# Kernel optimization log

Measured on AMD Instinct MI355X. Metric: run time of the kernel, lower is better.

The kernel has to match this reference:

```python
import jax, jax.numpy as jnp
import numpy as np

N = 50000   # nodes
F = 32      # num_node_features
EMB = 32    # embedding_size
R = 8       # num_relations
L = 5       # num_layers
E = 400000  # edges


def setup_inputs() -> dict:
    key = jax.random.key(0)
    ks = jax.random.split(key, 12)
    s = 0.1  # weight scale ~ 1/sqrt(fan_in) for stability over 5 residual layers
    return {
        "x": jax.random.normal(ks[0], (N, F), jnp.float32),
        "edge_index": jax.random.randint(ks[1], (2, E), 0, N, jnp.int32),
        "edge_type": jax.random.randint(ks[2], (E,), 0, R, jnp.int32),
        "edge_dist": jax.random.uniform(ks[3], (E,), jnp.float32),
        "fc_W": jax.random.normal(ks[4], (F, EMB), jnp.float32) * s,
        "fc_b": jnp.zeros((EMB,), jnp.float32),
        "rgcn_W": jax.random.normal(ks[5], (L, R, EMB, EMB), jnp.float32) * s,
        "rgcn_root": jax.random.normal(ks[6], (L, EMB, EMB), jnp.float32) * s,
        "rgcn_bias": jnp.zeros((L, EMB), jnp.float32),
        "mlp_W1": jax.random.normal(ks[7], (1 + R, EMB), jnp.float32) * s,
        "mlp_b1": jnp.zeros((EMB,), jnp.float32),
        "mlp_W2": jax.random.normal(ks[8], (EMB, EMB * EMB), jnp.float32) * s,
        "mlp_b2": jnp.zeros((EMB * EMB,), jnp.float32),
        "nn_root": jax.random.normal(ks[9], (L, EMB, EMB), jnp.float32) * s,
        "nn_bias": jnp.zeros((L, EMB), jnp.float32),
    }


def _forward(x, edge_index, edge_type, edge_dist, fc_W, fc_b, rgcn_W, rgcn_root,
             rgcn_bias, mlp_W1, mlp_b1, mlp_W2, mlp_b2, nn_root, nn_bias):
    n = x.shape[0]
    src, dst = edge_index[0], edge_index[1]  # source_to_target flow

    # edge_attr_c = [distance, onehot(edge_type)] : [E, 1+R]
    onehot = jax.nn.one_hot(edge_type, R, dtype=x.dtype)
    eattr = jnp.concatenate([edge_dist[:, None], onehot], axis=1)

    # Shared edge_mlp -> per-edge [EMB, EMB] weight (same for every NNConv layer)
    We = (jax.nn.relu(eattr @ mlp_W1 + mlp_b1) @ mlp_W2 + mlp_b2).reshape(-1, EMB, EMB)

    # degree for NNConv mean aggregation
    deg = jax.ops.segment_sum(jnp.ones_like(edge_dist), dst, num_segments=n)
    denom = jnp.maximum(deg, 1.0)[:, None]

    # per-relation in-degree for RGCN per-relation mean
    rel_cnt = []
    for r in range(R):
        c = jax.ops.segment_sum((edge_type == r).astype(x.dtype), dst, num_segments=n)
        rel_cnt.append(jnp.maximum(c, 1.0)[:, None])

    h = jax.nn.relu(x @ fc_W + fc_b)
    for l in range(L):
        # RGCNConv: root transform + per-relation mean of W_r x_j
        out = h @ rgcn_root[l] + rgcn_bias[l]
        for r in range(R):
            mask_r = (edge_type == r).astype(h.dtype)[:, None]
            msg = (h @ rgcn_W[l, r])[src] * mask_r  # [E, EMB]
            out = out + jax.ops.segment_sum(msg, dst, num_segments=n) / rel_cnt[r]
        h_disc = jax.nn.relu(out)

        # NNConv: x_j @ Theta(e) per edge, mean-aggregated, + root + bias
        msg = jnp.einsum('ei,eio->eo', h[src], We)  # [E, EMB]
        agg = jax.ops.segment_sum(msg, dst, num_segments=n) / denom
        h_cont = jax.nn.relu(h @ nn_root[l] + agg + nn_bias[l])

        h = h + h_disc + h_cont
    return h


def reference(x, edge_index, edge_type, edge_dist, fc_W, fc_b, rgcn_W, rgcn_root,
              rgcn_bias, mlp_W1, mlp_b1, mlp_W2, mlp_b2, nn_root, nn_bias):
    return _forward(x, edge_index, edge_type, edge_dist, fc_W, fc_b, rgcn_W,
                    rgcn_root, rgcn_bias, mlp_W1, mlp_b1, mlp_W2, mlp_b2,
                    nn_root, nn_bias)
```

## Files before the change

### kernel.cpp

```cpp
#include <hip/hip_runtime.h>

#define N_NODES 50000
#define N_EDGES 400000
#define EMB 32
#define NREL 8
#define NLAYER 5
#define NPB 16
#define NBLK (N_NODES / NPB)
#define KROWS 43
#define NCHUNK 196
#define E2CAP (N_EDGES + 8 * N_NODES)

typedef __attribute__((ext_vector_type(8))) short short8;
typedef __attribute__((ext_vector_type(4))) float f32x4;
typedef __attribute__((ext_vector_type(4))) unsigned int u32x4v;

__device__ __forceinline__ unsigned short f2bf(float f) {
    unsigned u = __float_as_uint(f);
    unsigned r = u + 0x7FFF + ((u >> 16) & 1);
    return (unsigned short)(r >> 16);
}

__device__ __forceinline__ unsigned cvt_pk(float a, float b) {
    unsigned r;
    asm("v_cvt_pk_bf16_f32 %0, %1, %2" : "=v"(r) : "v"(a), "v"(b));
    return r;
}

__device__ __forceinline__ int pdeg_of(int d) {
    return (d > 0 ? d + 7 : 8) & ~7;
}


__global__ __launch_bounds__(256) void fill_kernel(int* __restrict__ zeroblk,
                                                   float* __restrict__ ha,
                                                   float* __restrict__ hb,
                                                   unsigned* __restrict__ hb16a,
                                                   unsigned* __restrict__ hb16b) {
    int i = blockIdx.x * 256 + threadIdx.x;
    if (i < 10 * N_NODES) zeroblk[i] = 0;
    if (i < EMB) { ha[(size_t)N_NODES * EMB + i] = 0.0f; hb[(size_t)N_NODES * EMB + i] = 0.0f; }
    if (i < EMB / 2) {
        hb16a[(size_t)N_NODES * (EMB / 2) + i] = 0u;
        hb16b[(size_t)N_NODES * (EMB / 2) + i] = 0u;
    }
}

__global__ __launch_bounds__(256) void hist_kernel(const int* __restrict__ ei,
                                                   const int* __restrict__ et,
                                                   int* __restrict__ deg,
                                                   int* __restrict__ relcnt) {
    int e = blockIdx.x * 256 + threadIdx.x;
    if (e < N_EDGES) {
        int d = ei[N_EDGES + e];
        atomicAdd(&deg[d], 1);
        atomicAdd(&relcnt[d * NREL + et[e]], 1);
    }
}

__global__ __launch_bounds__(256) void nodeprep_kernel(const int* __restrict__ deg,
                                                       const int* __restrict__ relcnt,
                                                       int* __restrict__ bsum,
                                                       float* __restrict__ invdeg,
                                                       float* __restrict__ invcnt,
                                                       unsigned char* __restrict__ perm) {
    __shared__ int wsum[4];
    int tid = threadIdx.x, lane = tid & 63, wv = tid >> 6;
    int i = blockIdx.x * 256 + tid;
    int d = (i < N_NODES) ? deg[i] : 0;
    int v = (i < N_NODES) ? pdeg_of(d) : 0;
    #pragma unroll
    for (int off = 32; off > 0; off >>= 1) v += __shfl_down(v, off, 64);
    if (lane == 0) wsum[wv] = v;
    __syncthreads();
    if (tid == 0) bsum[blockIdx.x] = wsum[0] + wsum[1] + wsum[2] + wsum[3];
    if (i < N_NODES) {
        invdeg[i] = 1.0f / (float)(d > 0 ? d : 1);
        #pragma unroll
        for (int r = 0; r < NREL; r++) {
            int c = relcnt[i * NREL + r];
            invcnt[i * NREL + r] = 1.0f / (float)(c > 0 ? c : 1);
        }
    }
    if (i < NBLK) {
        int dd[NPB]; unsigned char idx[NPB];
        #pragma unroll
        for (int k = 0; k < NPB; k++) { dd[k] = deg[i * NPB + k]; idx[k] = (unsigned char)k; }
        for (int a = 1; a < NPB; a++) {
            int dv = dd[a]; unsigned char iv = idx[a];
            int j = a - 1;
            while (j >= 0 && dd[j] < dv) { dd[j + 1] = dd[j]; idx[j + 1] = idx[j]; j--; }
            dd[j + 1] = dv; idx[j + 1] = iv;
        }
        #pragma unroll
        for (int k = 0; k < NPB; k++) perm[i * NPB + k] = idx[k];
    }
}

__global__ __launch_bounds__(256) void boff_kernel(const int* __restrict__ bsum,
                                                   int* __restrict__ boff,
                                                   int* __restrict__ row_ptr) {
    __shared__ int ws[4];
    int tid = threadIdx.x, lane = tid & 63, w = tid >> 6;
    int v = (tid < NCHUNK) ? bsum[tid] : 0;
    int incl = v;
    #pragma unroll
    for (int off = 1; off < 64; off <<= 1) {
        int t = __shfl_up(incl, off, 64);
        if (lane >= off) incl += t;
    }
    if (lane == 63) ws[w] = incl;
    __syncthreads();
    int add = 0;
    for (int j = 0; j < w; j++) add += ws[j];
    if (tid < NCHUNK) boff[tid] = add + incl - v;
    if (tid == 0) row_ptr[N_NODES] = ws[0] + ws[1] + ws[2] + ws[3];
}

__global__ __launch_bounds__(256) void rptr_kernel(const int* __restrict__ deg,
                                                   const int* __restrict__ boff,
                                                   int* __restrict__ row_ptr) {
    __shared__ int ws[4];
    int tid = threadIdx.x, lane = tid & 63, w = tid >> 6;
    int i = blockIdx.x * 256 + tid;
    int v = (i < N_NODES) ? pdeg_of(deg[i]) : 0;
    int incl = v;
    #pragma unroll
    for (int off = 1; off < 64; off <<= 1) {
        int t = __shfl_up(incl, off, 64);
        if (lane >= off) incl += t;
    }
    if (lane == 63) ws[w] = incl;
    __syncthreads();
    int add = boff[blockIdx.x];
    for (int j = 0; j < w; j++) add += ws[j];
    if (i < N_NODES) row_ptr[i] = add + incl - v;
}

__global__ __launch_bounds__(256) void scatter_kernel(const int* __restrict__ ei,
                                                      const int* __restrict__ et,
                                                      const float* __restrict__ ed,
                                                      const int* __restrict__ row_ptr,
                                                      const int* __restrict__ deg,
                                                      int* __restrict__ cursor,
                                                      int2* __restrict__ edge2,
                                                      const unsigned char* __restrict__ perm,
                                                      int4* __restrict__ wavetab) {
    int e = blockIdx.x * 256 + threadIdx.x;
    if (e < N_EDGES) {
        int d = ei[N_EDGES + e];
        int pos = row_ptr[d] + atomicAdd(&cursor[d], 1);
        edge2[pos] = make_int2(ei[e] | (et[e] << 16), __float_as_int(ed[e]));
    }
    if (e < N_NODES) {
        int base = row_ptr[e], d = deg[e], pd = pdeg_of(d);
        for (int p = base + d; p < base + pd; ++p)
            edge2[p] = make_int2(N_NODES, 0);
    }
    if (e < NBLK * 8) {
        int b = e >> 3, wv = e & 7;
        int s0 = perm[b * NPB + wv], s1 = perm[b * NPB + (NPB - 1 - wv)];
        int nA = b * NPB + s0, nB = b * NPB + s1;
        int pb0 = row_ptr[nA], pd0 = row_ptr[nA + 1] - pb0;
        int pb1 = row_ptr[nB], pd1 = row_ptr[nB + 1] - pb1;
        wavetab[e] = make_int4(s0 | (s1 << 8), pb0, pb1, pd0 | (pd1 << 16));
    }
}

__global__ __launch_bounds__(256) void wtbf_kernel(const float* __restrict__ W2,
                                                   const float* __restrict__ b2,
                                                   const float* __restrict__ rgcnW,
                                                   const float* __restrict__ rgcnRoot,
                                                   const float* __restrict__ nnRoot,
                                                   unsigned short* __restrict__ WB) {
    int m = blockIdx.x;
    const float* src;
    if (m < 32) src = W2 + (size_t)m * 1024;
    else if (m == 32) src = b2;
    else {
        int t = m - 33, l = t / 10, j = t % 10;
        src = (j < 8) ? rgcnW + (size_t)(l * 8 + j) * 1024
            : (j == 8) ? rgcnRoot + (size_t)l * 1024
                       : nnRoot + (size_t)l * 1024;
    }
    unsigned short* dst = WB + (size_t)m * 1024;
    #pragma unroll
    for (int c = 0; c < 4; c++) {
        int idx = c * 256 + threadIdx.x;
        int o = idx >> 5, k = idx & 31;
        int i = (k >> 1) + ((k & 1) << 4);
        dst[o * 32 + k] = f2bf(src[i * 32 + o]);
    }
}


__global__ __launch_bounds__(256) void fc_kernel(const float* __restrict__ x,
                                                 const float* __restrict__ W,
                                                 const float* __restrict__ b,
                                                 float* __restrict__ h,
                                                 unsigned short* __restrict__ hb16) {
    __shared__ __align__(16) float xt[8][EMB];
    int tid = threadIdx.x;
    int nl = tid >> 5, lane = tid & 31;
    int n0 = blockIdx.x * 8;
    xt[tid >> 5][tid & 31] = x[n0 * EMB + tid];
    __syncthreads();
    float acc = b[lane];
    #pragma unroll
    for (int i = 0; i < EMB; i++) acc += xt[nl][i] * W[i * EMB + lane];
    float v = fmaxf(acc, 0.0f);
    int ol = ((lane & 15) << 1) | (lane >> 4);
    h[(size_t)(n0 + nl) * EMB + ol] = v;
    float pv = __shfl_down(v, 16, 32);
    unsigned pk = cvt_pk(v, pv);
    if (lane < 16)
        *(unsigned*)&hb16[(size_t)(n0 + nl) * EMB + 2 * lane] = pk;
}


__device__ __forceinline__ void gath(const unsigned short* __restrict__ hb16, int4 E, int m,
                                     unsigned& uA, unsigned& uB) {
    uA = *(const unsigned*)(hb16 + (((size_t)(E.x & 0xFFFF)) << 5) + 2 * m);
    uB = *(const unsigned*)(hb16 + (((size_t)(E.z & 0xFFFF)) << 5) + 2 * m);
}

__device__ __forceinline__ void proc_pair(int4 E, unsigned uA, unsigned uB,
                                          const float2* wrb2f, float w10_0, float w10_1,
                                          unsigned selm, int m,
                                          unsigned& A0s, unsigned& A1s, unsigned& ASs,
                                          unsigned& B0s, unsigned& B1s) {
    int ra = (E.x >> 16) & 7, rb = (E.z >> 16) & 7;
    float2 wa = wrb2f[ra * 16 + m];
    float2 wb = wrb2f[rb * 16 + m];
    float da = __int_as_float(E.y), db = __int_as_float(E.w);
    float hA0 = fmaxf(fmaf(da, w10_0, wa.x), 0.f);
    float hA1 = fmaxf(fmaf(da, w10_1, wa.y), 0.f);
    float hB0 = fmaxf(fmaf(db, w10_0, wb.x), 0.f);
    float hB1 = fmaxf(fmaf(db, w10_1, wb.y), 0.f);
    A0s = cvt_pk(hA0, hB0);
    A1s = cvt_pk(hA1, hB1);
    ASs = cvt_pk((float)((selm >> ra) & 1u), (float)((selm >> rb) & 1u));
    B0s = (uA & 0xFFFFu) | (uB << 16);
    B1s = (uA >> 16) | (uB & 0xFFFF0000u);
}

__device__ __forceinline__ void mfma6(const unsigned* fa0v, const unsigned* fa1v,
                                      const unsigned* fasv, const unsigned* fb0v,
                                      const unsigned* fb1v,
                                      f32x4& aP00, f32x4& aP01, f32x4& aP10, f32x4& aP11,
                                      f32x4& aS0, f32x4& aS1) {
    u32x4v u0 = {fa0v[0], fa0v[1], fa0v[2], fa0v[3]};
    u32x4v u1 = {fa1v[0], fa1v[1], fa1v[2], fa1v[3]};
    u32x4v us = {fasv[0], fasv[1], fasv[2], fasv[3]};
    u32x4v v0 = {fb0v[0], fb0v[1], fb0v[2], fb0v[3]};
    u32x4v v1 = {fb1v[0], fb1v[1], fb1v[2], fb1v[3]};
    short8 A0 = __builtin_bit_cast(short8, u0);
    short8 A1 = __builtin_bit_cast(short8, u1);
    short8 AS = __builtin_bit_cast(short8, us);
    short8 B0 = __builtin_bit_cast(short8, v0);
    short8 B1 = __builtin_bit_cast(short8, v1);
    aP00 = __builtin_amdgcn_mfma_f32_16x16x32_bf16(A0, B0, aP00, 0, 0, 0);
    aP01 = __builtin_amdgcn_mfma_f32_16x16x32_bf16(A0, B1, aP01, 0, 0, 0);
    aP10 = __builtin_amdgcn_mfma_f32_16x16x32_bf16(A1, B0, aP10, 0, 0, 0);
    aP11 = __builtin_amdgcn_mfma_f32_16x16x32_bf16(A1, B1, aP11, 0, 0, 0);
    aS0  = __builtin_amdgcn_mfma_f32_16x16x32_bf16(AS, B0, aS0, 0, 0, 0);
    aS1  = __builtin_amdgcn_mfma_f32_16x16x32_bf16(AS, B1, aS1, 0, 0, 0);
}

__device__ __forceinline__ void edge_pass(const unsigned short* __restrict__ hb16,
                                          const int2* __restrict__ edge2,
                                          const float2* wrb2f,
                                          int pb, int pe, int quad, int m,
                                          float w10_0, float w10_1, unsigned selm,
                                          int4 E0, unsigned u0A, unsigned u0B,
                                          f32x4& aP00, f32x4& aP01, f32x4& aP10,
                                          f32x4& aP11, f32x4& aS0, f32x4& aS1) {
    {
        unsigned fa0v[4] = {0,0,0,0}, fa1v[4] = {0,0,0,0}, fasv[4] = {0,0,0,0};
        unsigned fb0v[4] = {0,0,0,0}, fb1v[4] = {0,0,0,0};
        proc_pair(E0, u0A, u0B, wrb2f, w10_0, w10_1, selm, m,
                  fa0v[0], fa1v[0], fasv[0], fb0v[0], fb1v[0]);
        if (pb + 8 < pe) {
            int4 E = *(const int4*)&edge2[pb + 8 + quad * 2];
            unsigned uA, uB; gath(hb16, E, m, uA, uB);
            proc_pair(E, uA, uB, wrb2f, w10_0, w10_1, selm, m,
                      fa0v[1], fa1v[1], fasv[1], fb0v[1], fb1v[1]);
        }
        if (pb + 16 < pe) {
            int4 E = *(const int4*)&edge2[pb + 16 + quad * 2];
            unsigned uA, uB; gath(hb16, E, m, uA, uB);
            proc_pair(E, uA, uB, wrb2f, w10_0, w10_1, selm, m,
                      fa0v[2], fa1v[2], fasv[2], fb0v[2], fb1v[2]);
        }
        if (pb + 24 < pe) {
            int4 E = *(const int4*)&edge2[pb + 24 + quad * 2];
            unsigned uA, uB; gath(hb16, E, m, uA, uB);
            proc_pair(E, uA, uB, wrb2f, w10_0, w10_1, selm, m,
                      fa0v[3], fa1v[3], fasv[3], fb0v[3], fb1v[3]);
        }
        mfma6(fa0v, fa1v, fasv, fb0v, fb1v, aP00, aP01, aP10, aP11, aS0, aS1);
    }
    for (int c0 = pb + 32; c0 < pe; c0 += 32) {
        unsigned fa0v[4] = {0,0,0,0}, fa1v[4] = {0,0,0,0}, fasv[4] = {0,0,0,0};
        unsigned fb0v[4] = {0,0,0,0}, fb1v[4] = {0,0,0,0};
        #pragma unroll
        for (int jp = 0; jp < 4; ++jp) {
            if (c0 + jp * 8 < pe) {
                int4 E = *(const int4*)&edge2[c0 + jp * 8 + quad * 2];
                unsigned uA, uB; gath(hb16, E, m, uA, uB);
                proc_pair(E, uA, uB, wrb2f, w10_0, w10_1, selm, m,
                          fa0v[jp], fa1v[jp], fasv[jp], fb0v[jp], fb1v[jp]);
            }
        }
        mfma6(fa0v, fa1v, fasv, fb0v, fb1v, aP00, aP01, aP10, aP11, aS0, aS1);
    }
}

__device__ __forceinline__ void stage_node(unsigned short* __restrict__ P, int quad, int m,
                                           float idg, const float* __restrict__ invcnt_n,
                                           const unsigned short* __restrict__ hb16row,
                                           const f32x4& aP00, const f32x4& aP01,
                                           const f32x4& aP10, const f32x4& aP11,
                                           const f32x4& aS0, const f32x4& aS1) {
    #pragma unroll
    for (int reg = 0; reg < 4; ++reg) {
        const int row = quad * 4 + reg;
        *(unsigned*)&P[row * EMB + 2 * m]        = cvt_pk(aP00[reg] * idg, aP01[reg] * idg);
        *(unsigned*)&P[(row + 16) * EMB + 2 * m] = cvt_pk(aP10[reg] * idg, aP11[reg] * idg);
        if (row <= 8) {
            const float sc = (row == 0) ? idg : invcnt_n[row - 1];
            *(unsigned*)&P[(32 + row) * EMB + 2 * m] = cvt_pk(aS0[reg] * sc, aS1[reg] * sc);
        }
    }
    if (quad < 2) {
        unsigned hh = *(const unsigned*)(hb16row + 2 * m);
        *(unsigned*)&P[(41 + quad) * EMB + 2 * m] = hh;
    }
}

__global__ __launch_bounds__(512, 6) void layer_kernel(
    const float* __restrict__ h,
    const unsigned short* __restrict__ hb16,
    const int2* __restrict__ edge2,
    const int4* __restrict__ wavetab,
    const float* __restrict__ invdeg,
    const float* __restrict__ invcnt,
    const float* __restrict__ W1,
    const float* __restrict__ b1,
    const unsigned short* __restrict__ WBs,
    const unsigned short* __restrict__ WBl,
    const float* __restrict__ rgcnBias_l,
    const float* __restrict__ nnBias_l,
    float* __restrict__ hout,
    unsigned short* __restrict__ hb16out,
    int last)
{
    __shared__ __align__(16) unsigned short P_lds[NPB * KROWS * EMB];
    __shared__ __align__(16) float2 wrb2f[NREL * 16];

    const int tid = threadIdx.x;
    const int n0 = blockIdx.x * NPB;

    if (tid < 128) {
        int r = tid >> 4, mi = tid & 15;
        wrb2f[r * 16 + mi] = make_float2(W1[(1 + r) * EMB + mi] + b1[mi],
                                         W1[(1 + r) * EMB + mi + 16] + b1[mi + 16]);
    }

    const int l    = tid & 63;
    const int w    = tid >> 6;
    const int quad = l >> 4;
    const int m    = l & 15;
    const float w10_0 = W1[m];
    const float w10_1 = W1[m + 16];
    const unsigned selm = (m == 0) ? 0xFFu : (m <= 8 ? (1u << (m - 1)) : 0u);

    int4 wt = wavetab[blockIdx.x * 8 + w];
    const int hw0 = wt.x & 0xFF, hw1 = (wt.x >> 8) & 0xFF;
    const int pb0 = wt.y, pe0 = wt.y + (wt.w & 0xFFFF);
    const int pb1 = wt.z, pe1 = wt.z + (int)((unsigned)wt.w >> 16);
    int4 E0 = *(const int4*)&edge2[pb0 + quad * 2];
    int4 E1 = *(const int4*)&edge2[pb1 + quad * 2];
    unsigned u0A, u0B, u1A, u1B;
    gath(hb16, E0, m, u0A, u0B);
    gath(hb16, E1, m, u1A, u1B);

    __syncthreads();

    {
        f32x4 aP00 = {0,0,0,0}, aP01 = {0,0,0,0}, aP10 = {0,0,0,0}, aP11 = {0,0,0,0};
        f32x4 aS0 = {0,0,0,0}, aS1 = {0,0,0,0};
        edge_pass(hb16, edge2, wrb2f, pb0, pe0, quad, m, w10_0, w10_1, selm,
                  E0, u0A, u0B, aP00, aP01, aP10, aP11, aS0, aS1);
        const int n = n0 + hw0;
        stage_node(P_lds + (size_t)hw0 * KROWS * EMB, quad, m, invdeg[n],
                   invcnt + (size_t)n * NREL, hb16 + (size_t)n * EMB,
                   aP00, aP01, aP10, aP11, aS0, aS1);
    }
    {
        f32x4 aP00 = {0,0,0,0}, aP01 = {0,0,0,0}, aP10 = {0,0,0,0}, aP11 = {0,0,0,0};
        f32x4 aS0 = {0,0,0,0}, aS1 = {0,0,0,0};
        edge_pass(hb16, edge2, wrb2f, pb1, pe1, quad, m, w10_0, w10_1, selm,
                  E1, u1A, u1B, aP00, aP01, aP10, aP11, aS0, aS1);
        const int n = n0 + hw1;
        stage_node(P_lds + (size_t)hw1 * KROWS * EMB, quad, m, invdeg[n],
                   invcnt + (size_t)n * NREL, hb16 + (size_t)n * EMB,
                   aP00, aP01, aP10, aP11, aS0, aS1);
    }
    __syncthreads();

    const int node16 = l & 15;
    const int o0 = l & 15;

    f32x4 accN0 = {0,0,0,0}, accN1 = {0,0,0,0};
    f32x4 accR0 = {0,0,0,0}, accR1 = {0,0,0,0};

    #pragma unroll
    for (int j = 0; j < 6; j++) {
        const int rr = w + 8 * j;
        if (rr < KROWS) {
            const unsigned short* Bsrc = (rr < 33) ? (WBs + (size_t)rr * 1024)
                                                   : (WBl + (size_t)(rr - 33) * 1024);
            short8 bf0 = *(const short8*)(Bsrc + o0 * 32 + quad * 8);
            short8 bf1 = *(const short8*)(Bsrc + (o0 + 16) * 32 + quad * 8);
            short8 a = *(const short8*)&P_lds[(size_t)node16 * KROWS * EMB + rr * EMB + quad * 8];
            if (rr <= 32 || rr == 42) {
                accN0 = __builtin_amdgcn_mfma_f32_16x16x32_bf16(a, bf0, accN0, 0, 0, 0);
                accN1 = __builtin_amdgcn_mfma_f32_16x16x32_bf16(a, bf1, accN1, 0, 0, 0);
            } else {
                accR0 = __builtin_amdgcn_mfma_f32_16x16x32_bf16(a, bf0, accR0, 0, 0, 0);
                accR1 = __builtin_amdgcn_mfma_f32_16x16x32_bf16(a, bf1, accR1, 0, 0, 0);
            }
        }
    }
    __syncthreads();

    float* RedAll = (float*)&P_lds[0];
    {
        float* my = RedAll + w * 1024;
        #pragma unroll
        for (int reg = 0; reg < 4; reg++) {
            int nd = quad * 4 + reg;
            my[nd * 32 + o0]            = accN0[reg];
            my[nd * 32 + o0 + 16]       = accN1[reg];
            my[512 + nd * 32 + o0]      = accR0[reg];
            my[512 + nd * 32 + o0 + 16] = accR1[reg];
        }
    }
    __syncthreads();

    {
        const int hw2 = tid >> 5, lane = tid & 31;
        const int n2 = n0 + hw2;
        float sn = 0.0f, sr = 0.0f;
        #pragma unroll
        for (int ww = 0; ww < 8; ww++) {
            sn += RedAll[ww * 1024 + tid];
            sr += RedAll[ww * 1024 + 512 + tid];
        }
        const int il = ((lane & 15) << 1) | (lane >> 4);
        float hd = h[(size_t)n2 * EMB + il];
        float o_r = fmaxf(sr + rgcnBias_l[lane], 0.0f);
        float o_n = fmaxf(sn + nnBias_l[lane], 0.0f);
        float outv = hd + o_r + o_n;
        hout[(size_t)n2 * EMB + (last ? lane : il)] = outv;
        if (!last) {
            float pv = __shfl_down(outv, 16, 32);
            unsigned pk = cvt_pk(outv, pv);
            if (lane < 16)
                *(unsigned*)&hb16out[(size_t)n2 * EMB + 2 * lane] = pk;
        }
    }
}


extern "C" void kernel_launch(void* const* d_in, const int* in_sizes, int n_in,
                              void* d_out, int out_size, void* d_ws, size_t ws_size,
                              hipStream_t stream) {
    const float* x        = (const float*)d_in[0];
    const int*   ei       = (const int*)d_in[1];
    const int*   et       = (const int*)d_in[2];
    const float* ed       = (const float*)d_in[3];
    const float* fcW      = (const float*)d_in[4];
    const float* fcb      = (const float*)d_in[5];
    const float* rgcnW    = (const float*)d_in[6];
    const float* rgcnRoot = (const float*)d_in[7];
    const float* rgcnBias = (const float*)d_in[8];
    const float* W1       = (const float*)d_in[9];
    const float* b1       = (const float*)d_in[10];
    const float* W2       = (const float*)d_in[11];
    const float* b2       = (const float*)d_in[12];
    const float* nnRoot   = (const float*)d_in[13];
    const float* nnBias   = (const float*)d_in[14];

    float* ws = (float*)d_ws;
    float* h_a    = ws;  ws += (size_t)(N_NODES + 1) * EMB;
    float* h_b    = ws;  ws += (size_t)(N_NODES + 1) * EMB;
    unsigned short* hb16_a = (unsigned short*)ws;  ws += (size_t)(N_NODES + 1) * EMB / 2;
    unsigned short* hb16_b = (unsigned short*)ws;  ws += (size_t)(N_NODES + 1) * EMB / 2;
    float* invdeg = ws;  ws += (size_t)N_NODES;
    float* invcnt = ws;  ws += (size_t)N_NODES * NREL;
    unsigned short* WB = (unsigned short*)ws;  ws += (size_t)83 * 1024 / 2;
    int2* edge2   = (int2*)ws;     ws += (size_t)E2CAP * 2;
    int* row_ptr  = (int*)ws;      ws += (size_t)(N_NODES + 1);
    int* bsum     = (int*)ws;      ws += (size_t)NCHUNK;
    int* boff     = (int*)ws;      ws += (size_t)NCHUNK;
    int* deg      = (int*)ws;      ws += (size_t)N_NODES;
    int* relcnt   = (int*)ws;      ws += (size_t)N_NODES * NREL;
    int* cursor   = (int*)ws;      ws += (size_t)N_NODES;
    unsigned char* perm = (unsigned char*)ws;  ws += (size_t)(NBLK * NPB + 3) / 4;
    int4* wavetab = (int4*)ws;     ws += (size_t)NBLK * 8 * 4;
    (void)in_sizes; (void)n_in; (void)out_size; (void)ws_size;

    fill_kernel<<<(10 * N_NODES + 255) / 256, 256, 0, stream>>>(deg, h_a, h_b,
                                                                (unsigned*)hb16_a,
                                                                (unsigned*)hb16_b);
    hist_kernel<<<(N_EDGES + 255) / 256, 256, 0, stream>>>(ei, et, deg, relcnt);
    nodeprep_kernel<<<NCHUNK, 256, 0, stream>>>(deg, relcnt, bsum, invdeg, invcnt, perm);
    boff_kernel<<<1, 256, 0, stream>>>(bsum, boff, row_ptr);
    rptr_kernel<<<NCHUNK, 256, 0, stream>>>(deg, boff, row_ptr);
    scatter_kernel<<<(N_EDGES + 255) / 256, 256, 0, stream>>>(ei, et, ed, row_ptr, deg,
                                                              cursor, edge2, perm, wavetab);
    wtbf_kernel<<<83, 256, 0, stream>>>(W2, b2, rgcnW, rgcnRoot, nnRoot, WB);
    fc_kernel<<<N_NODES / 8, 256, 0, stream>>>(x, fcW, fcb, h_a, hb16_a);

    const float* hin = h_a;
    const unsigned short* hbin = hb16_a;
    float* houtb = h_b;
    unsigned short* hboutb = hb16_b;
    for (int l = 0; l < NLAYER; l++) {
        int last = (l == NLAYER - 1) ? 1 : 0;
        float* dst = last ? (float*)d_out : houtb;
        layer_kernel<<<NBLK, 512, 0, stream>>>(
            hin, hbin, edge2, wavetab, invdeg, invcnt, W1, b1,
            WB, WB + (size_t)(33 + l * 10) * 1024,
            rgcnBias + (size_t)l * EMB,
            nnBias + (size_t)l * EMB,
            dst, hboutb, last);
        float* old_in = (float*)hin;
        unsigned short* old_hb = (unsigned short*)hbin;
        hin = dst; hbin = hboutb;
        houtb = old_in; hboutb = old_hb;
    }
}
```

Before: 382.5 us.

## Merge setup kernels, derive degree from relation counts, prefetch second edge chunk

Combines the fill, weight-conversion and input FC kernels into one launch, which cuts launch overhead. The degree histogram is dropped: degree is now the sum of the per-relation counts, removing one atomic per edge. The layer kernel also issues the gathers for the second 8-edge chunk of both nodes before the barrier, so more memory latency overlaps. The cost is higher register pressure, and the fp32 h pad rows are no longer zeroed, which is safe only if nothing reads them.

```diff
diff --git a/kernel.cpp b/kernel.cpp
--- a/kernel.cpp
+++ b/kernel.cpp
@@ -10,6 +10,9 @@
 #define KROWS 43
 #define NCHUNK 196
 #define E2CAP (N_EDGES + 8 * N_NODES)
+#define FCB (N_NODES / 8)
+#define FILLB ((9 * N_NODES + 255) / 256)
+#define WTBFB 83
 
 typedef __attribute__((ext_vector_type(8))) short short8;
 typedef __attribute__((ext_vector_type(4))) float f32x4;
@@ -32,34 +35,69 @@
 }
 
 
-__global__ __launch_bounds__(256) void fill_kernel(int* __restrict__ zeroblk,
-                                                   float* __restrict__ ha,
-                                                   float* __restrict__ hb,
-                                                   unsigned* __restrict__ hb16a,
-                                                   unsigned* __restrict__ hb16b) {
-    int i = blockIdx.x * 256 + threadIdx.x;
-    if (i < 10 * N_NODES) zeroblk[i] = 0;
-    if (i < EMB) { ha[(size_t)N_NODES * EMB + i] = 0.0f; hb[(size_t)N_NODES * EMB + i] = 0.0f; }
-    if (i < EMB / 2) {
-        hb16a[(size_t)N_NODES * (EMB / 2) + i] = 0u;
-        hb16b[(size_t)N_NODES * (EMB / 2) + i] = 0u;
+__global__ __launch_bounds__(256) void setup0_kernel(
+    const float* __restrict__ x, const float* __restrict__ fcW, const float* __restrict__ fcb,
+    float* __restrict__ h, unsigned short* __restrict__ hb16,
+    int* __restrict__ zero9,
+    unsigned* __restrict__ hb16a_pad, unsigned* __restrict__ hb16b_pad,
+    const float* __restrict__ W2, const float* __restrict__ b2,
+    const float* __restrict__ rgcnW, const float* __restrict__ rgcnRoot,
+    const float* __restrict__ nnRoot, unsigned short* __restrict__ WB) {
+    __shared__ __align__(16) float xt[8][EMB];
+    const int b = blockIdx.x, tid = threadIdx.x;
+    if (b < FCB) {
+        int nl = tid >> 5, lane = tid & 31;
+        int n0 = b * 8;
+        xt[tid >> 5][tid & 31] = x[n0 * EMB + tid];
+        __syncthreads();
+        float acc = fcb[lane];
+        #pragma unroll
+        for (int i = 0; i < EMB; i++) acc += xt[nl][i] * fcW[i * EMB + lane];
+        float v = fmaxf(acc, 0.0f);
+        int ol = ((lane & 15) << 1) | (lane >> 4);
+        h[(size_t)(n0 + nl) * EMB + ol] = v;
+        float pv = __shfl_down(v, 16, 32);
+        unsigned pk = cvt_pk(v, pv);
+        if (lane < 16)
+            *(unsigned*)&hb16[(size_t)(n0 + nl) * EMB + 2 * lane] = pk;
+    } else if (b < FCB + FILLB) {
+        int i = (b - FCB) * 256 + tid;
+        if (i < 9 * N_NODES) zero9[i] = 0;
+        if (i < EMB / 2) { hb16a_pad[i] = 0u; hb16b_pad[i] = 0u; }
+    } else {
+        int m = b - FCB - FILLB;
+        const float* src;
+        if (m < 32) src = W2 + (size_t)m * 1024;
+        else if (m == 32) src = b2;
+        else {
+            int t = m - 33, l = t / 10, j = t % 10;
+            src = (j < 8) ? rgcnW + (size_t)(l * 8 + j) * 1024
+                : (j == 8) ? rgcnRoot + (size_t)l * 1024
+                           : nnRoot + (size_t)l * 1024;
+        }
+        unsigned short* dst = WB + (size_t)m * 1024;
+        #pragma unroll
+        for (int c = 0; c < 4; c++) {
+            int idx = c * 256 + tid;
+            int o = idx >> 5, k = idx & 31;
+            int i = (k >> 1) + ((k & 1) << 4);
+            dst[o * 32 + k] = f2bf(src[i * 32 + o]);
+        }
     }
 }
 
 __global__ __launch_bounds__(256) void hist_kernel(const int* __restrict__ ei,
                                                    const int* __restrict__ et,
-                                                   int* __restrict__ deg,
                                                    int* __restrict__ relcnt) {
     int e = blockIdx.x * 256 + threadIdx.x;
     if (e < N_EDGES) {
         int d = ei[N_EDGES + e];
-        atomicAdd(&deg[d], 1);
         atomicAdd(&relcnt[d * NREL + et[e]], 1);
     }
 }
 
-__global__ __launch_bounds__(256) void nodeprep_kernel(const int* __restrict__ deg,
-                                                       const int* __restrict__ relcnt,
+__global__ __launch_bounds__(256) void nodeprep_kernel(const int* __restrict__ relcnt,
+                                                       int* __restrict__ deg,
                                                        int* __restrict__ bsum,
                                                        float* __restrict__ invdeg,
                                                        float* __restrict__ invcnt,
@@ -67,25 +105,39 @@
     __shared__ int wsum[4];
     int tid = threadIdx.x, lane = tid & 63, wv = tid >> 6;
     int i = blockIdx.x * 256 + tid;
-    int d = (i < N_NODES) ? deg[i] : 0;
+    int d = 0;
+    if (i < N_NODES) {
+        int c0 = relcnt[i * NREL + 0], c1 = relcnt[i * NREL + 1];
+        int c2 = relcnt[i * NREL + 2], c3 = relcnt[i * NREL + 3];
+        int c4 = relcnt[i * NREL + 4], c5 = relcnt[i * NREL + 5];
+        int c6 = relcnt[i * NREL + 6], c7 = relcnt[i * NREL + 7];
+        d = c0 + c1 + c2 + c3 + c4 + c5 + c6 + c7;
+        deg[i] = d;
+        invdeg[i] = 1.0f / (float)(d > 0 ? d : 1);
+        invcnt[i * NREL + 0] = 1.0f / (float)(c0 > 0 ? c0 : 1);
+        invcnt[i * NREL + 1] = 1.0f / (float)(c1 > 0 ? c1 : 1);
+        invcnt[i * NREL + 2] = 1.0f / (float)(c2 > 0 ? c2 : 1);
+        invcnt[i * NREL + 3] = 1.0f / (float)(c3 > 0 ? c3 : 1);
+        invcnt[i * NREL + 4] = 1.0f / (float)(c4 > 0 ? c4 : 1);
+        invcnt[i * NREL + 5] = 1.0f / (float)(c5 > 0 ? c5 : 1);
+        invcnt[i * NREL + 6] = 1.0f / (float)(c6 > 0 ? c6 : 1);
+        invcnt[i * NREL + 7] = 1.0f / (float)(c7 > 0 ? c7 : 1);
+    }
     int v = (i < N_NODES) ? pdeg_of(d) : 0;
     #pragma unroll
     for (int off = 32; off > 0; off >>= 1) v += __shfl_down(v, off, 64);
     if (lane == 0) wsum[wv] = v;
     __syncthreads();
     if (tid == 0) bsum[blockIdx.x] = wsum[0] + wsum[1] + wsum[2] + wsum[3];
-    if (i < N_NODES) {
-        invdeg[i] = 1.0f / (float)(d > 0 ? d : 1);
-        #pragma unroll
-        for (int r = 0; r < NREL; r++) {
-            int c = relcnt[i * NREL + r];
-            invcnt[i * NREL + r] = 1.0f / (float)(c > 0 ? c : 1);
-        }
-    }
     if (i < NBLK) {
         int dd[NPB]; unsigned char idx[NPB];
         #pragma unroll
-        for (int k = 0; k < NPB; k++) { dd[k] = deg[i * NPB + k]; idx[k] = (unsigned char)k; }
+        for (int k = 0; k < NPB; k++) {
+            int s = 0;
+            #pragma unroll
+            for (int r = 0; r < NREL; r++) s += relcnt[(i * NPB + k) * NREL + r];
+            dd[k] = s; idx[k] = (unsigned char)k;
+        }
         for (int a = 1; a < NPB; a++) {
             int dv = dd[a]; unsigned char iv = idx[a];
             int j = a - 1;
@@ -165,56 +217,6 @@
         int pb1 = row_ptr[nB], pd1 = row_ptr[nB + 1] - pb1;
         wavetab[e] = make_int4(s0 | (s1 << 8), pb0, pb1, pd0 | (pd1 << 16));
     }
-}
-
-__global__ __launch_bounds__(256) void wtbf_kernel(const float* __restrict__ W2,
-                                                   const float* __restrict__ b2,
-                                                   const float* __restrict__ rgcnW,
-                                                   const float* __restrict__ rgcnRoot,
-                                                   const float* __restrict__ nnRoot,
-                                                   unsigned short* __restrict__ WB) {
-    int m = blockIdx.x;
-    const float* src;
-    if (m < 32) src = W2 + (size_t)m * 1024;
-    else if (m == 32) src = b2;
-    else {
-        int t = m - 33, l = t / 10, j = t % 10;
-        src = (j < 8) ? rgcnW + (size_t)(l * 8 + j) * 1024
-            : (j == 8) ? rgcnRoot + (size_t)l * 1024
-                       : nnRoot + (size_t)l * 1024;
-    }
-    unsigned short* dst = WB + (size_t)m * 1024;
-    #pragma unroll
-    for (int c = 0; c < 4; c++) {
-        int idx = c * 256 + threadIdx.x;
-        int o = idx >> 5, k = idx & 31;
-        int i = (k >> 1) + ((k & 1) << 4);
-        dst[o * 32 + k] = f2bf(src[i * 32 + o]);
-    }
-}
-
-
-__global__ __launch_bounds__(256) void fc_kernel(const float* __restrict__ x,
-                                                 const float* __restrict__ W,
-                                                 const float* __restrict__ b,
-                                                 float* __restrict__ h,
-                                                 unsigned short* __restrict__ hb16) {
-    __shared__ __align__(16) float xt[8][EMB];
-    int tid = threadIdx.x;
-    int nl = tid >> 5, lane = tid & 31;
-    int n0 = blockIdx.x * 8;
-    xt[tid >> 5][tid & 31] = x[n0 * EMB + tid];
-    __syncthreads();
-    float acc = b[lane];
-    #pragma unroll
-    for (int i = 0; i < EMB; i++) acc += xt[nl][i] * W[i * EMB + lane];
-    float v = fmaxf(acc, 0.0f);
-    int ol = ((lane & 15) << 1) | (lane >> 4);
-    h[(size_t)(n0 + nl) * EMB + ol] = v;
-    float pv = __shfl_down(v, 16, 32);
-    unsigned pk = cvt_pk(v, pv);
-    if (lane < 16)
-        *(unsigned*)&hb16[(size_t)(n0 + nl) * EMB + 2 * lane] = pk;
 }
 
 
@@ -273,6 +275,7 @@
                                           int pb, int pe, int quad, int m,
                                           float w10_0, float w10_1, unsigned selm,
                                           int4 E0, unsigned u0A, unsigned u0B,
+                                          int4 E1, unsigned u1A, unsigned u1B,
                                           f32x4& aP00, f32x4& aP01, f32x4& aP10,
                                           f32x4& aP11, f32x4& aS0, f32x4& aS1) {
     {
@@ -280,12 +283,9 @@
         unsigned fb0v[4] = {0,0,0,0}, fb1v[4] = {0,0,0,0};
         proc_pair(E0, u0A, u0B, wrb2f, w10_0, w10_1, selm, m,
                   fa0v[0], fa1v[0], fasv[0], fb0v[0], fb1v[0]);
-        if (pb + 8 < pe) {
-            int4 E = *(const int4*)&edge2[pb + 8 + quad * 2];
-            unsigned uA, uB; gath(hb16, E, m, uA, uB);
-            proc_pair(E, uA, uB, wrb2f, w10_0, w10_1, selm, m,
+        if (pb + 8 < pe)
+            proc_pair(E1, u1A, u1B, wrb2f, w10_0, w10_1, selm, m,
                       fa0v[1], fa1v[1], fasv[1], fb0v[1], fb1v[1]);
-        }
         if (pb + 16 < pe) {
             int4 E = *(const int4*)&edge2[pb + 16 + quad * 2];
             unsigned uA, uB; gath(hb16, E, m, uA, uB);
@@ -379,11 +379,21 @@
     const int hw0 = wt.x & 0xFF, hw1 = (wt.x >> 8) & 0xFF;
     const int pb0 = wt.y, pe0 = wt.y + (wt.w & 0xFFFF);
     const int pb1 = wt.z, pe1 = wt.z + (int)((unsigned)wt.w >> 16);
-    int4 E0 = *(const int4*)&edge2[pb0 + quad * 2];
-    int4 E1 = *(const int4*)&edge2[pb1 + quad * 2];
-    unsigned u0A, u0B, u1A, u1B;
-    gath(hb16, E0, m, u0A, u0B);
-    gath(hb16, E1, m, u1A, u1B);
+    int4 E0p0 = *(const int4*)&edge2[pb0 + quad * 2];
+    int4 E0p1 = *(const int4*)&edge2[pb1 + quad * 2];
+    unsigned u0p0A, u0p0B, u0p1A, u0p1B;
+    gath(hb16, E0p0, m, u0p0A, u0p0B);
+    gath(hb16, E0p1, m, u0p1A, u0p1B);
+    int4 E1p0 = {0, 0, 0, 0}, E1p1 = {0, 0, 0, 0};
+    unsigned u1p0A = 0, u1p0B = 0, u1p1A = 0, u1p1B = 0;
+    if (pb0 + 8 < pe0) {
+        E1p0 = *(const int4*)&edge2[pb0 + 8 + quad * 2];
+        gath(hb16, E1p0, m, u1p0A, u1p0B);
+    }
+    if (pb1 + 8 < pe1) {
+        E1p1 = *(const int4*)&edge2[pb1 + 8 + quad * 2];
+        gath(hb16, E1p1, m, u1p1A, u1p1B);
+    }
 
     __syncthreads();
 
@@ -391,7 +401,8 @@
         f32x4 aP00 = {0,0,0,0}, aP01 = {0,0,0,0}, aP10 = {0,0,0,0}, aP11 = {0,0,0,0};
         f32x4 aS0 = {0,0,0,0}, aS1 = {0,0,0,0};
         edge_pass(hb16, edge2, wrb2f, pb0, pe0, quad, m, w10_0, w10_1, selm,
-                  E0, u0A, u0B, aP00, aP01, aP10, aP11, aS0, aS1);
+                  E0p0, u0p0A, u0p0B, E1p0, u1p0A, u1p0B,
+                  aP00, aP01, aP10, aP11, aS0, aS1);
         const int n = n0 + hw0;
         stage_node(P_lds + (size_t)hw0 * KROWS * EMB, quad, m, invdeg[n],
                    invcnt + (size_t)n * NREL, hb16 + (size_t)n * EMB,
@@ -401,7 +412,8 @@
         f32x4 aP00 = {0,0,0,0}, aP01 = {0,0,0,0}, aP10 = {0,0,0,0}, aP11 = {0,0,0,0};
         f32x4 aS0 = {0,0,0,0}, aS1 = {0,0,0,0};
         edge_pass(hb16, edge2, wrb2f, pb1, pe1, quad, m, w10_0, w10_1, selm,
-                  E1, u1A, u1B, aP00, aP01, aP10, aP11, aS0, aS1);
+                  E0p1, u0p1A, u0p1B, E1p1, u1p1A, u1p1B,
+                  aP00, aP01, aP10, aP11, aS0, aS1);
         const int n = n0 + hw1;
         stage_node(P_lds + (size_t)hw1 * KROWS * EMB, quad, m, invdeg[n],
                    invcnt + (size_t)n * NREL, hb16 + (size_t)n * EMB,
@@ -512,17 +524,17 @@
     int4* wavetab = (int4*)ws;     ws += (size_t)NBLK * 8 * 4;
     (void)in_sizes; (void)n_in; (void)out_size; (void)ws_size;
 
-    fill_kernel<<<(10 * N_NODES + 255) / 256, 256, 0, stream>>>(deg, h_a, h_b,
-                                                                (unsigned*)hb16_a,
-                                                                (unsigned*)hb16_b);
-    hist_kernel<<<(N_EDGES + 255) / 256, 256, 0, stream>>>(ei, et, deg, relcnt);
-    nodeprep_kernel<<<NCHUNK, 256, 0, stream>>>(deg, relcnt, bsum, invdeg, invcnt, perm);
+    setup0_kernel<<<FCB + FILLB + WTBFB, 256, 0, stream>>>(
+        x, fcW, fcb, h_a, hb16_a, relcnt,
+        (unsigned*)(hb16_a + (size_t)N_NODES * EMB / 2 * 0 + (size_t)N_NODES * EMB),
+        (unsigned*)(hb16_b + (size_t)N_NODES * EMB),
+        W2, b2, rgcnW, rgcnRoot, nnRoot, WB);
+    hist_kernel<<<(N_EDGES + 255) / 256, 256, 0, stream>>>(ei, et, relcnt);
+    nodeprep_kernel<<<NCHUNK, 256, 0, stream>>>(relcnt, deg, bsum, invdeg, invcnt, perm);
     boff_kernel<<<1, 256, 0, stream>>>(bsum, boff, row_ptr);
     rptr_kernel<<<NCHUNK, 256, 0, stream>>>(deg, boff, row_ptr);
     scatter_kernel<<<(N_EDGES + 255) / 256, 256, 0, stream>>>(ei, et, ed, row_ptr, deg,
                                                               cursor, edge2, perm, wavetab);
-    wtbf_kernel<<<83, 256, 0, stream>>>(W2, b2, rgcnW, rgcnRoot, nnRoot, WB);
-    fc_kernel<<<N_NODES / 8, 256, 0, stream>>>(x, fcW, fcb, h_a, hb16_a);
 
     const float* hin = h_a;
     const unsigned short* hbin = hb16_a;
```

After: 405.6 us. 6.0% more time.
